# Performance work log

Hardware: AMD Instinct MI355X
Metric: run time of the kernel (lower is better)

## Reference

```python
import jax, jax.numpy as jnp
import numpy as np

SIZE = 896      # GRU hidden size
HALF = SIZE // 2
BINS = 256      # 2**(bits/2), bits=16
B, T = 16, 1000


def _scale(t):
    # [0, BINS-1] ints -> [-1, 1] floats
    return t.astype(jnp.float32) / ((BINS - 1) / 2.0) - 1.0


def setup_inputs() -> dict:
    key = jax.random.key(0)
    ks = jax.random.split(key, 13)
    s = 0.05
    return {
        "conditional": jax.random.normal(ks[0], (B, T, 3, SIZE), jnp.float32),
        "gru_input_bias": jax.random.normal(ks[1], (3 * SIZE,), jnp.float32) * s,
        "W_h": jax.random.normal(ks[2], (3 * SIZE, SIZE), jnp.float32) * s,   # project_hidden
        "b_h": jax.random.normal(ks[3], (3 * SIZE,), jnp.float32) * s,
        "W_ci": jax.random.normal(ks[4], (3 * HALF, 2), jnp.float32) * s,     # project_coarse_input
        "b_ci": jax.random.normal(ks[5], (3 * HALF,), jnp.float32) * s,
        "W_fi": jax.random.normal(ks[6], (3 * HALF, 3), jnp.float32) * s,     # project_fine_input
        "b_fi": jax.random.normal(ks[7], (3 * HALF,), jnp.float32) * s,
        "W_bc": jax.random.normal(ks[8], (BINS, HALF), jnp.float32) * s,      # to_bins_coarse
        "b_bc": jax.random.normal(ks[9], (BINS,), jnp.float32) * s,
        "W_bf": jax.random.normal(ks[10], (BINS, HALF), jnp.float32) * s,     # to_bins_fine
        "b_bf": jax.random.normal(ks[11], (BINS,), jnp.float32) * s,
    }


def reference(conditional, gru_input_bias, W_h, b_h, W_ci, b_ci, W_fi, b_fi,
              W_bc, b_bc, W_bf, b_bf):
    # Fold input-GRU biases into the conditional (as the torch code does in-place)
    cond = conditional + gru_input_bias.reshape(3, SIZE)  # [B,T,3,SIZE]
    # split each gate into coarse/fine halves and regroup as (r,u,e)
    cc = jnp.concatenate([cond[:, :, 0, :HALF], cond[:, :, 1, :HALF], cond[:, :, 2, :HALF]], -1)
    cf = jnp.concatenate([cond[:, :, 0, HALF:], cond[:, :, 1, HALF:], cond[:, :, 2, HALF:]], -1)
    cc = jnp.transpose(cc, (1, 0, 2))  # [T,B,3*HALF]
    cf = jnp.transpose(cf, (1, 0, 2))
    sample_key = jax.random.key(1)

    # initial state: split_signal(0) -> coarse=fine=0 -> scaled to -1
    init = (-jnp.ones((B, 1), jnp.float32), -jnp.ones((B, 1), jnp.float32),
            jnp.zeros((B, HALF), jnp.float32), jnp.zeros((B, HALF), jnp.float32))

    def step(carry, xs):
        cv, fv, ch, fh = carry
        ccond, fcond, t = xs
        k1, k2 = jax.random.split(jax.random.fold_in(sample_key, t))
        hidden = jnp.concatenate([ch, fh], 1)                   # [B,SIZE]
        hp = hidden @ W_h.T + b_h                               # [B,3*SIZE]
        hcr, hfr, hcu, hfu, hce, hfe = jnp.split(hp, 6, axis=1)
        h_cru = jnp.concatenate([hcr, hcu], 1)
        h_fru = jnp.concatenate([hfr, hfu], 1)
        # coarse half-step
        cin = jnp.concatenate([cv, fv], 1)                      # [B,2]
        cp = cin @ W_ci.T + b_ci + ccond                        # [B,3*HALF]
        ru = jax.nn.sigmoid(cp[:, :SIZE] + h_cru)
        r, u = jnp.split(ru, 2, axis=1)
        e = jnp.tanh(r * hce + cp[:, SIZE:])
        ch = u * ch + (1.0 - u) * e
        logits_c = ch @ W_bc.T + b_bc                           # [B,BINS]
        sc = jax.random.categorical(k1, jax.nn.log_softmax(logits_c, axis=1))
        cv = _scale(sc)[:, None]
        # fine half-step
        fin = jnp.concatenate([cin, cv], 1)                     # [B,3]
        fp = fin @ W_fi.T + b_fi + fcond
        ru = jax.nn.sigmoid(fp[:, :SIZE] + h_fru)
        r, u = jnp.split(ru, 2, axis=1)
        e = jnp.tanh(r * hfe + fp[:, SIZE:])
        fh = u * fh + (1.0 - u) * e
        logits_f = fh @ W_bf.T + b_bf
        sf = jax.random.categorical(k2, jax.nn.log_softmax(logits_f, axis=1))
        fv = _scale(sf)[:, None]
        return (cv, fv, ch, fh), (sc, sf)

    (cv, fv, ch, fh), (oc, of) = jax.lax.scan(step, init, (cc, cf, jnp.arange(T)))
    hidden = jnp.concatenate([ch, fh], 1)
    return oc.T, of.T, hidden  # [B,T] int, [B,T] int, [B,SIZE]
```

## Files before the change

kernel.cpp:

```cpp
#include <hip/hip_runtime.h>
#include <stdint.h>

#define BB 16
#define TT 1000
#define SZ 896
#define HF 448
#define NC 112
#define NWG 240
#define LDS_FLOATS 30112
#define LDS_BYTES (LDS_FLOATS * 4)

typedef float f32x4 __attribute__((ext_vector_type(4)));
typedef float f32x2 __attribute__((ext_vector_type(2)));

__device__ float g_hid[2 * BB * SZ];
__device__ float g_hpf4[HF * BB * 4];
__device__ uint32_t g_cdone[NC * 16];
__device__ uint32_t g_fhd[BB * 16];
__device__ uint32_t g_sfd[BB * 16];
__device__ unsigned long long g_afl[BB * 4 * 8];
__device__ unsigned long long g_bfl[BB * 4 * 8];

__device__ __forceinline__ void cload4x4(const float* p, f32x4& a0, f32x4& a1, f32x4& a2, f32x4& a3) {
  asm volatile(
      "global_load_dwordx4 %0, %4, off sc0 sc1\n\t"
      "global_load_dwordx4 %1, %4, off offset:16 sc0 sc1\n\t"
      "global_load_dwordx4 %2, %4, off offset:32 sc0 sc1\n\t"
      "global_load_dwordx4 %3, %4, off offset:48 sc0 sc1\n\t"
      "s_waitcnt vmcnt(0)"
      : "=&v"(a0), "=&v"(a1), "=&v"(a2), "=&v"(a3) : "v"(p) : "memory");
}
__device__ __forceinline__ f32x4 cload1x4(const float* p) {
  f32x4 a;
  asm volatile("global_load_dwordx4 %0, %1, off sc0 sc1\n\ts_waitcnt vmcnt(0)"
               : "=&v"(a) : "v"(p) : "memory");
  return a;
}
__device__ __forceinline__ void cstore1d(float* p, float v) {
  asm volatile("global_store_dword %0, %1, off sc0 sc1\n\ts_waitcnt vmcnt(0)"
               :: "v"(p), "v"(v) : "memory");
}
__device__ __forceinline__ void cstore4d(float* p, f32x4 v) {
  asm volatile("global_store_dwordx4 %0, %1, off sc0 sc1\n\ts_waitcnt vmcnt(0)"
               :: "v"(p), "v"(v) : "memory");
}
__device__ __forceinline__ void cstore1u_nw(uint32_t* p, uint32_t v) {
  asm volatile("global_store_dword %0, %1, off sc0 sc1" :: "v"(p), "v"(v) : "memory");
}
__device__ __forceinline__ void cstore2u_nw(unsigned long long* p, f32x2 v) {
  asm volatile("global_store_dwordx2 %0, %1, off sc0 sc1" :: "v"(p), "v"(v) : "memory");
}

__device__ __forceinline__ void waitFlag(uint32_t* f, uint32_t target) {
  while (__hip_atomic_load(f, __ATOMIC_RELAXED, __HIP_MEMORY_SCOPE_AGENT) < target)
    __builtin_amdgcn_s_sleep(1);
}
__device__ __forceinline__ void waitFlagA(uint32_t* f, uint32_t target) {
  while (__hip_atomic_load(f, __ATOMIC_RELAXED, __HIP_MEMORY_SCOPE_AGENT) < target)
    __builtin_amdgcn_s_sleep(2);
}
__device__ __forceinline__ unsigned long long waitFlag64(unsigned long long* f, uint32_t tag) {
  unsigned long long u;
  while ((uint32_t)((u = __hip_atomic_load(f, __ATOMIC_RELAXED, __HIP_MEMORY_SCOPE_AGENT)) >> 48) < tag)
    __builtin_amdgcn_s_sleep(1);
  return u;
}
__device__ __forceinline__ uint32_t waitFlagHi8(uint32_t* f, uint32_t tag) {
  uint32_t v;
  while (((v = __hip_atomic_load(f, __ATOMIC_RELAXED, __HIP_MEMORY_SCOPE_AGENT)) >> 8) < tag)
    __builtin_amdgcn_s_sleep(1);
  return v;
}

__device__ __forceinline__ uint32_t rotl32(uint32_t v, int d) {
  return (v << d) | (v >> (32 - d));
}

__device__ __forceinline__ uint2 tf2(uint32_t k0, uint32_t k1, uint32_t x0, uint32_t x1) {
  const uint32_t k2 = k0 ^ k1 ^ 0x1BD11BDAu;
  x0 += k0; x1 += k1;
  x0 += x1; x1 = rotl32(x1,13); x1 ^= x0;
  x0 += x1; x1 = rotl32(x1,15); x1 ^= x0;
  x0 += x1; x1 = rotl32(x1,26); x1 ^= x0;
  x0 += x1; x1 = rotl32(x1, 6); x1 ^= x0;
  x0 += k1; x1 += k2 + 1u;
  x0 += x1; x1 = rotl32(x1,17); x1 ^= x0;
  x0 += x1; x1 = rotl32(x1,29); x1 ^= x0;
  x0 += x1; x1 = rotl32(x1,16); x1 ^= x0;
  x0 += x1; x1 = rotl32(x1,24); x1 ^= x0;
  x0 += k2; x1 += k0 + 2u;
  x0 += x1; x1 = rotl32(x1,13); x1 ^= x0;
  x0 += x1; x1 = rotl32(x1,15); x1 ^= x0;
  x0 += x1; x1 = rotl32(x1,26); x1 ^= x0;
  x0 += x1; x1 = rotl32(x1, 6); x1 ^= x0;
  x0 += k0; x1 += k1 + 3u;
  x0 += x1; x1 = rotl32(x1,17); x1 ^= x0;
  x0 += x1; x1 = rotl32(x1,29); x1 ^= x0;
  x0 += x1; x1 = rotl32(x1,16); x1 ^= x0;
  x0 += x1; x1 = rotl32(x1,24); x1 ^= x0;
  x0 += k1; x1 += k2 + 4u;
  x0 += x1; x1 = rotl32(x1,13); x1 ^= x0;
  x0 += x1; x1 = rotl32(x1,15); x1 ^= x0;
  x0 += x1; x1 = rotl32(x1,26); x1 ^= x0;
  x0 += x1; x1 = rotl32(x1, 6); x1 ^= x0;
  x0 += k2; x1 += k0 + 5u;
  return make_uint2(x0, x1);
}

__device__ __forceinline__ float gumbel_bits(uint32_t bits) {
  const float tiny = 1.17549435e-38f;
  float f = __uint_as_float((bits >> 9) | 0x3f800000u) - 1.0f;
  float u = fmaxf(tiny, f + tiny);
  return -logf(-logf(u));
}

__device__ __forceinline__ void logits64(const float* __restrict__ wlds,
                                         const float* __restrict__ vec,
                                         float* __restrict__ plds, int tid) {
  const int w = tid >> 6, lane = tid & 63;
  float a = 0.f;
  const float* wp = wlds + (56 * w) * 65 + lane;
  const float* cp = vec + 56 * w;
#pragma unroll 8
  for (int ii = 0; ii < 56; ++ii)
    a = fmaf(cp[ii], wp[ii * 65], a);
  plds[(w << 6) | lane] = a;
}

__global__ __launch_bounds__(256, 1) void wavernn_init() {
  const int idx = blockIdx.x * 256 + threadIdx.x;
  g_hid[idx] = 0.f;
  if (idx < NC * 16) g_cdone[idx] = 0u;
  if (idx < BB * 16) { g_fhd[idx] = 0u; g_sfd[idx] = 0u; }
  if (idx < BB * 4 * 8) { g_afl[idx] = 0ull; g_bfl[idx] = 0ull; }
}

__global__ __launch_bounds__(512, 1) void wavernn_main(
    const float* __restrict__ cond, const float* __restrict__ gib,
    const float* __restrict__ W_h,  const float* __restrict__ b_h,
    const float* __restrict__ W_ci, const float* __restrict__ b_ci,
    const float* __restrict__ W_fi, const float* __restrict__ b_fi,
    const float* __restrict__ W_bc, const float* __restrict__ b_bc,
    const float* __restrict__ W_bf, const float* __restrict__ b_bf,
    float* __restrict__ out) {
  extern __shared__ float smem[];
  const int wg = blockIdx.x, tid = threadIdx.x;

  if (wg < NC) {
    float* hlds = smem;
    int* smcv = (int*)(smem + 14400);
    int* smfv = (int*)(smem + 14416);
    const int wave = tid >> 6, lane = tid & 63;
    const int l32 = lane >> 1, b2 = lane & 1;
    const int tp = wave >> 2;
    const int chan = (wg << 2) | (wave & 3);
    const int rb = tp ? (HF + chan) : chan;
    float4 w[3][7];
    float brow[3];
#pragma unroll
    for (int r = 0; r < 3; ++r) {
      const int row = r * SZ + rb;
      brow[r] = b_h[row];
#pragma unroll
      for (int m = 0; m < 7; ++m)
        w[r][m] = *(const float4*)&W_h[(size_t)row * SZ + 4 * l32 + 128 * m];
    }
    float wci0[3], wci1[3], bcie[3];
    if (tp == 0) {
#pragma unroll
      for (int g = 0; g < 3; ++g) {
        const int rr = g * HF + chan;
        wci0[g] = W_ci[2 * rr]; wci1[g] = W_ci[2 * rr + 1];
        bcie[g] = b_ci[rr] + gib[g * SZ + chan];
      }
    }
    float pc0 = 0.f, pc1 = 0.f, pc2 = 0.f;
    if (tp == 0 && lane < 16) {
      const size_t base = (((size_t)lane * TT) * 3) * SZ + chan;
      pc0 = cond[base]; pc1 = cond[base + SZ]; pc2 = cond[base + 2 * SZ];
    }
    float chreg = 0.f;
    const int r16 = tid & 15, c28 = tid >> 4;

    for (int t = 0; t < TT; ++t) {
      const int p = (t & 1) ^ 1;
      const int q = t & 1;
      if (tid < NC) waitFlagA(&g_cdone[tid * 16], (uint32_t)t);
      __syncthreads();
      if (c28 < 28) {
        const float* src = g_hid + (size_t)p * BB * SZ + r16 * SZ + c28 * 16;
        f32x4 a0, a1, a2, a3;
        cload4x4(src, a0, a1, a2, a3);
        float* dst = hlds + r16 * 900 + c28 * 16;
        *(f32x4*)(dst) = a0; *(f32x4*)(dst + 4) = a1;
        *(f32x4*)(dst + 8) = a2; *(f32x4*)(dst + 12) = a3;
      }
      __syncthreads();
      float acc[3][8];
#pragma unroll
      for (int r = 0; r < 3; ++r)
#pragma unroll
        for (int i = 0; i < 8; ++i) acc[r][i] = 0.f;
#pragma unroll
      for (int i = 0; i < 8; ++i) {
        const int b = b2 + 2 * i;
        const float* hb = hlds + b * 900 + 4 * l32;
        const float4 h0 = *(const float4*)(hb);
        const float4 h1 = *(const float4*)(hb + 128);
        const float4 h2 = *(const float4*)(hb + 256);
#pragma unroll
        for (int r = 0; r < 3; ++r) {
          float s = acc[r][i];
          s = fmaf(w[r][0].x, h0.x, s); s = fmaf(w[r][0].y, h0.y, s);
          s = fmaf(w[r][0].z, h0.z, s); s = fmaf(w[r][0].w, h0.w, s);
          s = fmaf(w[r][1].x, h1.x, s); s = fmaf(w[r][1].y, h1.y, s);
          s = fmaf(w[r][1].z, h1.z, s); s = fmaf(w[r][1].w, h1.w, s);
          s = fmaf(w[r][2].x, h2.x, s); s = fmaf(w[r][2].y, h2.y, s);
          s = fmaf(w[r][2].z, h2.z, s); s = fmaf(w[r][2].w, h2.w, s);
          acc[r][i] = s;
        }
        if (l32 < 16) {
          const float4 h3 = *(const float4*)(hb + 384);
#pragma unroll
          for (int r = 0; r < 3; ++r) {
            float s = acc[r][i];
            s = fmaf(w[r][3].x, h3.x, s); s = fmaf(w[r][3].y, h3.y, s);
            s = fmaf(w[r][3].z, h3.z, s); s = fmaf(w[r][3].w, h3.w, s);
            acc[r][i] = s;
          }
        }
      }
      if (tid < BB) {
        const uint32_t v = waitFlagHi8(&g_fhd[tid * 16], (uint32_t)t);
        smcv[tid] = (int)(v & 255u);
      }
      __syncthreads();
      if (c28 < 28) {
        const float* src = g_hid + (size_t)p * BB * SZ + r16 * SZ + HF + c28 * 16;
        f32x4 a0, a1, a2, a3;
        cload4x4(src, a0, a1, a2, a3);
        float* dst = hlds + r16 * 900 + HF + c28 * 16;
        *(f32x4*)(dst) = a0; *(f32x4*)(dst + 4) = a1;
        *(f32x4*)(dst + 8) = a2; *(f32x4*)(dst + 12) = a3;
      }
      __syncthreads();
#pragma unroll
      for (int i = 0; i < 8; ++i) {
        const int b = b2 + 2 * i;
        const float* hb = hlds + b * 900 + 4 * l32;
        if (l32 >= 16) {
          const float4 h3 = *(const float4*)(hb + 384);
#pragma unroll
          for (int r = 0; r < 3; ++r) {
            float s = acc[r][i];
            s = fmaf(w[r][3].x, h3.x, s); s = fmaf(w[r][3].y, h3.y, s);
            s = fmaf(w[r][3].z, h3.z, s); s = fmaf(w[r][3].w, h3.w, s);
            acc[r][i] = s;
          }
        }
        const float4 h4 = *(const float4*)(hb + 512);
        const float4 h5 = *(const float4*)(hb + 640);
        const float4 h6 = *(const float4*)(hb + 768);
#pragma unroll
        for (int r = 0; r < 3; ++r) {
          float s = acc[r][i];
          s = fmaf(w[r][4].x, h4.x, s); s = fmaf(w[r][4].y, h4.y, s);
          s = fmaf(w[r][4].z, h4.z, s); s = fmaf(w[r][4].w, h4.w, s);
          s = fmaf(w[r][5].x, h5.x, s); s = fmaf(w[r][5].y, h5.y, s);
          s = fmaf(w[r][5].z, h5.z, s); s = fmaf(w[r][5].w, h5.w, s);
          s = fmaf(w[r][6].x, h6.x, s); s = fmaf(w[r][6].y, h6.y, s);
          s = fmaf(w[r][6].z, h6.z, s); s = fmaf(w[r][6].w, h6.w, s);
          acc[r][i] = s;
        }
      }
#pragma unroll
      for (int r = 0; r < 3; ++r)
#pragma unroll
        for (int i = 0; i < 8; ++i) {
          float v = acc[r][i];
          v += __shfl_xor(v, 2);
          v += __shfl_xor(v, 4);
          v += __shfl_xor(v, 8);
          v += __shfl_xor(v, 16);
          v += __shfl_xor(v, 32);
          acc[r][i] = v;
        }
      if (tid < BB) {
        const uint32_t v = waitFlagHi8(&g_sfd[tid * 16], (uint32_t)t);
        smfv[tid] = (int)(v & 255u);
      }
      __syncthreads();
      if (lane < 16) {
        const int bb = lane, i = lane >> 1;
        const float s0 = acc[0][i] + brow[0];
        const float s1 = acc[1][i] + brow[1];
        const float s2 = acc[2][i] + brow[2];
        if (tp == 0) {
          const float cvv = (float)smcv[bb] / 127.5f - 1.0f;
          const float fvv = (float)smfv[bb] / 127.5f - 1.0f;
          const float cp0 = fmaf(cvv, wci0[0], fmaf(fvv, wci1[0], bcie[0])) + pc0;
          const float cp1 = fmaf(cvv, wci0[1], fmaf(fvv, wci1[1], bcie[1])) + pc1;
          const float cp2 = fmaf(cvv, wci0[2], fmaf(fvv, wci1[2], bcie[2])) + pc2;
          const float rg = 1.f / (1.f + expf(-(cp0 + s0)));
          const float ug = 1.f / (1.f + expf(-(cp1 + s1)));
          const float eg = tanhf(fmaf(rg, s2, cp2));
          const float chn = ug * chreg + (1.f - ug) * eg;
          chreg = chn;
          cstore1d(&g_hid[(size_t)q * BB * SZ + bb * SZ + chan], chn);
        } else {
          f32x4 hv; hv.x = s0; hv.y = s1; hv.z = s2; hv.w = 0.f;
          cstore4d(&g_hpf4[((size_t)chan * 16 + bb) * 4], hv);
        }
      }
      __syncthreads();
      if (tid == 0) cstore1u_nw(&g_cdone[wg * 16], (uint32_t)(t + 1));
      if (tp == 0 && lane < 16 && t + 1 < TT) {
        const size_t base = (((size_t)lane * TT + (t + 1)) * 3) * SZ + chan;
        pc0 = cond[base]; pc1 = cond[base + SZ]; pc2 = cond[base + 2 * SZ];
      }
    }
  } else {
    const int swg = wg - NC;
    const int b = swg >> 3;
    const int role = (swg >> 2) & 1;
    const int k = swg & 3;
    float* wlds = smem;
    float* vlds = smem + 29120;
    float* plds = smem + 29568;
    float* aS = smem + 30080;
    int*   aI = (int*)(smem + 30084);
    float* bS = smem + 30088;
    int*   bI = (int*)(smem + 30092);
    {
      const float* Wm = role ? W_bf : W_bc;
      for (int i = tid; i < HF * 64; i += 512) {
        const int bn = i / HF, kk = i - bn * HF;
        wlds[kk * 65 + bn] = Wm[(size_t)(64 * k + bn) * HF + kk];
      }
    }
    const float* bias = role ? b_bf : b_bc;
    float wf0[3], wf1[3], wf2[3], bfe[3];
    float cp0 = 0.f, cp1 = 0.f, cp2 = 0.f;
    if (role == 1 && tid < HF) {
#pragma unroll
      for (int g = 0; g < 3; ++g) {
        const int rr = g * HF + tid;
        wf0[g] = W_fi[3 * rr]; wf1[g] = W_fi[3 * rr + 1]; wf2[g] = W_fi[3 * rr + 2];
        bfe[g] = b_fi[rr] + gib[g * SZ + HF + tid];
      }
      const size_t cbase = (((size_t)b * TT) * 3) * SZ + HF + tid;
      cp0 = cond[cbase]; cp1 = cond[cbase + SZ]; cp2 = cond[cbase + 2 * SZ];
      vlds[tid] = 0.f;
    }
    __syncthreads();
    float cvO = -1.f, fvO = -1.f;

    for (int t = 0; t < TT; ++t) {
      const int q = t & 1;
      const uint2 kf = tf2(0u, 1u, 0u, (uint32_t)t);
      float gub = 0.f;
      if (tid < 64) {
        const uint2 kk = role ? tf2(kf.x, kf.y, 0u, 1u) : tf2(kf.x, kf.y, 0u, 0u);
        const uint2 o = tf2(kk.x, kk.y, 0u, (uint32_t)(b * 256 + 64 * k + tid));
        gub = gumbel_bits(o.x ^ o.y);
      }
      if (role == 0) {
        if (tid < NC) waitFlag(&g_cdone[tid * 16], (uint32_t)(t + 1));
        __syncthreads();
        if (tid < 112) {
          const f32x4 v = cload1x4(g_hid + (size_t)q * BB * SZ + b * SZ + 4 * tid);
          *(f32x4*)&vlds[4 * tid] = v;
        }
        __syncthreads();
        logits64(wlds, vlds, plds, tid);
        __syncthreads();
        if (tid < 64) {
          const float p0 = plds[tid],       p1 = plds[64 + tid];
          const float p2 = plds[128 + tid], p3 = plds[192 + tid];
          const float p4 = plds[256 + tid], p5 = plds[320 + tid];
          const float p6 = plds[384 + tid], p7 = plds[448 + tid];
          const float sum = ((p0 + p1) + (p2 + p3)) + ((p4 + p5) + (p6 + p7));
          float s = (sum + bias[64 * k + tid]) + gub;
          int idx = 64 * k + tid;
#pragma unroll
          for (int m = 1; m < 64; m <<= 1) {
            const float so = __shfl_xor(s, m);
            const int io = __shfl_xor(idx, m);
            if (so > s || (so == s && io < idx)) { s = so; idx = io; }
          }
          if (tid == 0) {
            f32x2 v; v.x = s;
            v.y = __uint_as_float(((uint32_t)(t + 1) << 16) | ((uint32_t)idx << 8));
            cstore2u_nw(&g_afl[(b * 4 + k) * 8], v);
          }
        }
      } else {
        if (tid < NC) waitFlag(&g_cdone[tid * 16], (uint32_t)(t + 1));
        __syncthreads();
        f32x4 hp = {0.f, 0.f, 0.f, 0.f};
        if (tid < HF) hp = cload1x4(g_hpf4 + ((size_t)tid * 16 + b) * 4);
        if (tid >= 448 && tid < 452) {
          const unsigned long long u = waitFlag64(&g_afl[(b * 4 + (tid - 448)) * 8], (uint32_t)(t + 1));
          aS[tid - 448] = __uint_as_float((uint32_t)u);
          aI[tid - 448] = (int)((u >> 40) & 255u);
        }
        __syncthreads();
        float ms = aS[0]; int sc = aI[0];
#pragma unroll
        for (int m = 1; m < 4; ++m) {
          const float so = aS[m]; const int io = aI[m];
          if (so > ms || (so == ms && io < sc)) { ms = so; sc = io; }
        }
        const float cvNew = (float)sc / 127.5f - 1.0f;
        if (tid < HF) {
          const float fp0 = fmaf(cvO, wf0[0], fmaf(fvO, wf1[0], fmaf(cvNew, wf2[0], bfe[0]))) + cp0;
          const float fp1 = fmaf(cvO, wf0[1], fmaf(fvO, wf1[1], fmaf(cvNew, wf2[1], bfe[1]))) + cp1;
          const float fp2 = fmaf(cvO, wf0[2], fmaf(fvO, wf1[2], fmaf(cvNew, wf2[2], bfe[2]))) + cp2;
          const float fhold = vlds[tid];
          const float rg = 1.f / (1.f + expf(-(fp0 + hp.x)));
          const float ug = 1.f / (1.f + expf(-(fp1 + hp.y)));
          const float eg = tanhf(fmaf(rg, hp.z, fp2));
          vlds[tid] = ug * fhold + (1.f - ug) * eg;
        }
        __syncthreads();
        if (k == 0) {
          if (tid < 112)
            cstore4d(&g_hid[(size_t)q * BB * SZ + b * SZ + HF + 4 * tid], *(f32x4*)&vlds[4 * tid]);
          __syncthreads();
          if (tid == 0) cstore1u_nw(&g_fhd[b * 16], ((uint32_t)(t + 1) << 8) | (uint32_t)sc);
        }
        logits64(wlds, vlds, plds, tid);
        __syncthreads();
        if (tid < 64) {
          const float p0 = plds[tid],       p1 = plds[64 + tid];
          const float p2 = plds[128 + tid], p3 = plds[192 + tid];
          const float p4 = plds[256 + tid], p5 = plds[320 + tid];
          const float p6 = plds[384 + tid], p7 = plds[448 + tid];
          const float sum = ((p0 + p1) + (p2 + p3)) + ((p4 + p5) + (p6 + p7));
          float s = (sum + bias[64 * k + tid]) + gub;
          int idx = 64 * k + tid;
#pragma unroll
          for (int m = 1; m < 64; m <<= 1) {
            const float so = __shfl_xor(s, m);
            const int io = __shfl_xor(idx, m);
            if (so > s || (so == s && io < idx)) { s = so; idx = io; }
          }
          if (tid == 0) {
            f32x2 v; v.x = s;
            v.y = __uint_as_float(((uint32_t)(t + 1) << 16) | ((uint32_t)idx << 8));
            cstore2u_nw(&g_bfl[(b * 4 + k) * 8], v);
          }
        }
        if (tid >= 448 && tid < 452) {
          const unsigned long long u = waitFlag64(&g_bfl[(b * 4 + (tid - 448)) * 8], (uint32_t)(t + 1));
          bS[tid - 448] = __uint_as_float((uint32_t)u);
          bI[tid - 448] = (int)((u >> 40) & 255u);
        }
        __syncthreads();
        float msf = bS[0]; int sf = bI[0];
#pragma unroll
        for (int m = 1; m < 4; ++m) {
          const float so = bS[m]; const int io = bI[m];
          if (so > msf || (so == msf && io < sf)) { msf = so; sf = io; }
        }
        if (k == 0 && tid == 0) {
          out[b * TT + t] = (float)sc;
          out[BB * TT + b * TT + t] = (float)sf;
          cstore1u_nw(&g_sfd[b * 16], ((uint32_t)(t + 1) << 8) | (uint32_t)sf);
        }
        cvO = cvNew; fvO = (float)sf / 127.5f - 1.0f;
        if (tid < HF && t + 1 < TT) {
          const size_t cbase = (((size_t)b * TT + (t + 1)) * 3) * SZ + HF + tid;
          cp0 = cond[cbase]; cp1 = cond[cbase + SZ]; cp2 = cond[cbase + 2 * SZ];
        }
      }
    }
    if (k == 0) {
      if (role == 0) {
        if (tid < HF) out[2 * BB * TT + (size_t)b * SZ + tid] = vlds[tid];
      } else {
        if (tid < HF) out[2 * BB * TT + (size_t)b * SZ + HF + tid] = vlds[tid];
      }
    }
  }
}

extern "C" void kernel_launch(void* const* d_in, const int* in_sizes, int n_in,
                              void* d_out, int out_size, void* d_ws, size_t ws_size,
                              hipStream_t stream) {
  (void)in_sizes; (void)n_in; (void)out_size; (void)d_ws; (void)ws_size;
  const float* cond = (const float*)d_in[0];
  const float* gib  = (const float*)d_in[1];
  const float* W_h  = (const float*)d_in[2];
  const float* b_h  = (const float*)d_in[3];
  const float* W_ci = (const float*)d_in[4];
  const float* b_ci = (const float*)d_in[5];
  const float* W_fi = (const float*)d_in[6];
  const float* b_fi = (const float*)d_in[7];
  const float* W_bc = (const float*)d_in[8];
  const float* b_bc = (const float*)d_in[9];
  const float* W_bf = (const float*)d_in[10];
  const float* b_bf = (const float*)d_in[11];
  float* out = (float*)d_out;
  static int attr_done = 0;
  (void)attr_done;
  hipFuncSetAttribute((const void*)wavernn_main,
                      hipFuncAttributeMaxDynamicSharedMemorySize, LDS_BYTES);
  wavernn_init<<<NC, 256, 0, stream>>>();
  wavernn_main<<<NWG, 512, LDS_BYTES, stream>>>(cond, gib, W_h, b_h, W_ci, b_ci,
                                                W_fi, b_fi, W_bc, b_bc, W_bf, b_bf, out);
}
```

Baseline: 12.15 ms.

## Move coarse GRU gate update from matvec workgroups into per-batch coarse-sampling workgroups

The coarse hidden-state gate math moves out of the hidden-projection workgroups and into the per-batch coarse-role workgroups, mirroring the fine path. Projection workgroups now only write pre-activations (g_hpc4/g_hpf4) and signal completion. They no longer wait for the sampled coarse and fine values each step, which removes a dependency from the critical chain. Coarse workgroups now read the previous fine sample from the fine argmax flags and publish the coarse hidden state through a new per-batch ready flag. The cost is more cross-workgroup flag traffic and more coordination inside the sampling workgroups.

```diff
diff --git a/kernel.cpp b/kernel.cpp
--- a/kernel.cpp
+++ b/kernel.cpp
@@ -14,10 +14,11 @@
 typedef float f32x2 __attribute__((ext_vector_type(2)));
 
 __device__ float g_hid[2 * BB * SZ];
-__device__ float g_hpf4[HF * BB * 4];
+__device__ float g_hpc4[BB * HF * 4];
+__device__ float g_hpf4[BB * HF * 4];
 __device__ uint32_t g_cdone[NC * 16];
-__device__ uint32_t g_fhd[BB * 16];
-__device__ uint32_t g_sfd[BB * 16];
+__device__ uint32_t g_chrdy[BB * 16];
+__device__ uint32_t g_fhrdy[BB * 16];
 __device__ unsigned long long g_afl[BB * 4 * 8];
 __device__ unsigned long long g_bfl[BB * 4 * 8];
 
@@ -36,10 +37,6 @@
                : "=&v"(a) : "v"(p) : "memory");
   return a;
 }
-__device__ __forceinline__ void cstore1d(float* p, float v) {
-  asm volatile("global_store_dword %0, %1, off sc0 sc1\n\ts_waitcnt vmcnt(0)"
-               :: "v"(p), "v"(v) : "memory");
-}
 __device__ __forceinline__ void cstore4d(float* p, f32x4 v) {
   asm volatile("global_store_dwordx4 %0, %1, off sc0 sc1\n\ts_waitcnt vmcnt(0)"
                :: "v"(p), "v"(v) : "memory");
@@ -64,12 +61,6 @@
   while ((uint32_t)((u = __hip_atomic_load(f, __ATOMIC_RELAXED, __HIP_MEMORY_SCOPE_AGENT)) >> 48) < tag)
     __builtin_amdgcn_s_sleep(1);
   return u;
-}
-__device__ __forceinline__ uint32_t waitFlagHi8(uint32_t* f, uint32_t tag) {
-  uint32_t v;
-  while (((v = __hip_atomic_load(f, __ATOMIC_RELAXED, __HIP_MEMORY_SCOPE_AGENT)) >> 8) < tag)
-    __builtin_amdgcn_s_sleep(1);
-  return v;
 }
 
 __device__ __forceinline__ uint32_t rotl32(uint32_t v, int d) {
@@ -131,7 +122,7 @@
   const int idx = blockIdx.x * 256 + threadIdx.x;
   g_hid[idx] = 0.f;
   if (idx < NC * 16) g_cdone[idx] = 0u;
-  if (idx < BB * 16) { g_fhd[idx] = 0u; g_sfd[idx] = 0u; }
+  if (idx < BB * 16) { g_chrdy[idx] = 0u; g_fhrdy[idx] = 0u; }
   if (idx < BB * 4 * 8) { g_afl[idx] = 0ull; g_bfl[idx] = 0ull; }
 }
 
@@ -148,8 +139,6 @@
 
   if (wg < NC) {
     float* hlds = smem;
-    int* smcv = (int*)(smem + 14400);
-    int* smfv = (int*)(smem + 14416);
     const int wave = tid >> 6, lane = tid & 63;
     const int l32 = lane >> 1, b2 = lane & 1;
     const int tp = wave >> 2;
@@ -165,27 +154,11 @@
       for (int m = 0; m < 7; ++m)
         w[r][m] = *(const float4*)&W_h[(size_t)row * SZ + 4 * l32 + 128 * m];
     }
-    float wci0[3], wci1[3], bcie[3];
-    if (tp == 0) {
-#pragma unroll
-      for (int g = 0; g < 3; ++g) {
-        const int rr = g * HF + chan;
-        wci0[g] = W_ci[2 * rr]; wci1[g] = W_ci[2 * rr + 1];
-        bcie[g] = b_ci[rr] + gib[g * SZ + chan];
-      }
-    }
-    float pc0 = 0.f, pc1 = 0.f, pc2 = 0.f;
-    if (tp == 0 && lane < 16) {
-      const size_t base = (((size_t)lane * TT) * 3) * SZ + chan;
-      pc0 = cond[base]; pc1 = cond[base + SZ]; pc2 = cond[base + 2 * SZ];
-    }
-    float chreg = 0.f;
     const int r16 = tid & 15, c28 = tid >> 4;
 
     for (int t = 0; t < TT; ++t) {
       const int p = (t & 1) ^ 1;
-      const int q = t & 1;
-      if (tid < NC) waitFlagA(&g_cdone[tid * 16], (uint32_t)t);
+      if (tid < BB) waitFlagA(&g_chrdy[tid * 16], (uint32_t)t);
       __syncthreads();
       if (c28 < 28) {
         const float* src = g_hid + (size_t)p * BB * SZ + r16 * SZ + c28 * 16;
@@ -230,10 +203,7 @@
           }
         }
       }
-      if (tid < BB) {
-        const uint32_t v = waitFlagHi8(&g_fhd[tid * 16], (uint32_t)t);
-        smcv[tid] = (int)(v & 255u);
-      }
+      if (tid < BB) waitFlag(&g_fhrdy[tid * 16], (uint32_t)t);
       __syncthreads();
       if (c28 < 28) {
         const float* src = g_hid + (size_t)p * BB * SZ + r16 * SZ + HF + c28 * 16;
@@ -285,39 +255,18 @@
           v += __shfl_xor(v, 32);
           acc[r][i] = v;
         }
-      if (tid < BB) {
-        const uint32_t v = waitFlagHi8(&g_sfd[tid * 16], (uint32_t)t);
-        smfv[tid] = (int)(v & 255u);
-      }
-      __syncthreads();
       if (lane < 16) {
         const int bb = lane, i = lane >> 1;
-        const float s0 = acc[0][i] + brow[0];
-        const float s1 = acc[1][i] + brow[1];
-        const float s2 = acc[2][i] + brow[2];
-        if (tp == 0) {
-          const float cvv = (float)smcv[bb] / 127.5f - 1.0f;
-          const float fvv = (float)smfv[bb] / 127.5f - 1.0f;
-          const float cp0 = fmaf(cvv, wci0[0], fmaf(fvv, wci1[0], bcie[0])) + pc0;
-          const float cp1 = fmaf(cvv, wci0[1], fmaf(fvv, wci1[1], bcie[1])) + pc1;
-          const float cp2 = fmaf(cvv, wci0[2], fmaf(fvv, wci1[2], bcie[2])) + pc2;
-          const float rg = 1.f / (1.f + expf(-(cp0 + s0)));
-          const float ug = 1.f / (1.f + expf(-(cp1 + s1)));
-          const float eg = tanhf(fmaf(rg, s2, cp2));
-          const float chn = ug * chreg + (1.f - ug) * eg;
-          chreg = chn;
-          cstore1d(&g_hid[(size_t)q * BB * SZ + bb * SZ + chan], chn);
-        } else {
-          f32x4 hv; hv.x = s0; hv.y = s1; hv.z = s2; hv.w = 0.f;
-          cstore4d(&g_hpf4[((size_t)chan * 16 + bb) * 4], hv);
-        }
+        f32x4 hv;
+        hv.x = acc[0][i] + brow[0];
+        hv.y = acc[1][i] + brow[1];
+        hv.z = acc[2][i] + brow[2];
+        hv.w = 0.f;
+        float* dst = (tp ? g_hpf4 : g_hpc4) + ((size_t)bb * HF + chan) * 4;
+        cstore4d(dst, hv);
       }
       __syncthreads();
       if (tid == 0) cstore1u_nw(&g_cdone[wg * 16], (uint32_t)(t + 1));
-      if (tp == 0 && lane < 16 && t + 1 < TT) {
-        const size_t base = (((size_t)lane * TT + (t + 1)) * 3) * SZ + chan;
-        pc0 = cond[base]; pc1 = cond[base + SZ]; pc2 = cond[base + 2 * SZ];
-      }
     }
   } else {
     const int swg = wg - NC;
@@ -339,21 +288,30 @@
       }
     }
     const float* bias = role ? b_bf : b_bc;
-    float wf0[3], wf1[3], wf2[3], bfe[3];
-    float cp0 = 0.f, cp1 = 0.f, cp2 = 0.f;
-    if (role == 1 && tid < HF) {
-#pragma unroll
-      for (int g = 0; g < 3; ++g) {
-        const int rr = g * HF + tid;
-        wf0[g] = W_fi[3 * rr]; wf1[g] = W_fi[3 * rr + 1]; wf2[g] = W_fi[3 * rr + 2];
-        bfe[g] = b_fi[rr] + gib[g * SZ + HF + tid];
-      }
-      const size_t cbase = (((size_t)b * TT) * 3) * SZ + HF + tid;
-      cp0 = cond[cbase]; cp1 = cond[cbase + SZ]; cp2 = cond[cbase + 2 * SZ];
+    float gw0[3], gw1[3], gw2[3], gbe[3], pc[3];
+    if (tid < HF) {
+      if (role == 0) {
+#pragma unroll
+        for (int g = 0; g < 3; ++g) {
+          const int rr = g * HF + tid;
+          gw0[g] = W_ci[2 * rr]; gw1[g] = W_ci[2 * rr + 1]; gw2[g] = 0.f;
+          gbe[g] = b_ci[rr] + gib[g * SZ + tid];
+          pc[g] = cond[(((size_t)b * TT) * 3 + g) * SZ + tid];
+        }
+      } else {
+#pragma unroll
+        for (int g = 0; g < 3; ++g) {
+          const int rr = g * HF + tid;
+          gw0[g] = W_fi[3 * rr]; gw1[g] = W_fi[3 * rr + 1]; gw2[g] = W_fi[3 * rr + 2];
+          gbe[g] = b_fi[rr] + gib[g * SZ + HF + tid];
+          pc[g] = cond[(((size_t)b * TT) * 3 + g) * SZ + HF + tid];
+        }
+      }
       vlds[tid] = 0.f;
     }
     __syncthreads();
-    float cvO = -1.f, fvO = -1.f;
+    float cvO = -1.f;
+    float fvO = -1.f;
 
     for (int t = 0; t < TT; ++t) {
       const int q = t & 1;
@@ -365,13 +323,40 @@
         gub = gumbel_bits(o.x ^ o.y);
       }
       if (role == 0) {
+        if (t > 0 && tid >= 452 && tid < 456) {
+          const unsigned long long u = waitFlag64(&g_bfl[(b * 4 + (tid - 452)) * 8], (uint32_t)t);
+          bS[tid - 452] = __uint_as_float((uint32_t)u);
+          bI[tid - 452] = (int)((u >> 40) & 255u);
+        }
         if (tid < NC) waitFlag(&g_cdone[tid * 16], (uint32_t)(t + 1));
         __syncthreads();
-        if (tid < 112) {
-          const f32x4 v = cload1x4(g_hid + (size_t)q * BB * SZ + b * SZ + 4 * tid);
-          *(f32x4*)&vlds[4 * tid] = v;
-        }
-        __syncthreads();
+        float fvv = -1.f;
+        if (t > 0) {
+          float ms = bS[0]; int sf = bI[0];
+#pragma unroll
+          for (int m = 1; m < 4; ++m) {
+            const float so = bS[m]; const int io = bI[m];
+            if (so > ms || (so == ms && io < sf)) { ms = so; sf = io; }
+          }
+          fvv = (float)sf / 127.5f - 1.0f;
+        }
+        if (tid < HF) {
+          const f32x4 hp = cload1x4(&g_hpc4[((size_t)b * HF + tid) * 4]);
+          const float cp0 = fmaf(cvO, gw0[0], fmaf(fvv, gw1[0], gbe[0])) + pc[0];
+          const float cp1 = fmaf(cvO, gw0[1], fmaf(fvv, gw1[1], gbe[1])) + pc[1];
+          const float cp2 = fmaf(cvO, gw0[2], fmaf(fvv, gw1[2], gbe[2])) + pc[2];
+          const float rg = 1.f / (1.f + expf(-(cp0 + hp.x)));
+          const float ug = 1.f / (1.f + expf(-(cp1 + hp.y)));
+          const float eg = tanhf(fmaf(rg, hp.z, cp2));
+          vlds[tid] = ug * vlds[tid] + (1.f - ug) * eg;
+        }
+        __syncthreads();
+        if (k == 0) {
+          if (tid < 112)
+            cstore4d(&g_hid[(size_t)q * BB * SZ + b * SZ + 4 * tid], *(f32x4*)&vlds[4 * tid]);
+          __syncthreads();
+          if (tid == 0) cstore1u_nw(&g_chrdy[b * 16], (uint32_t)(t + 1));
+        }
         logits64(wlds, vlds, plds, tid);
         __syncthreads();
         if (tid < 64) {
@@ -394,17 +379,38 @@
             cstore2u_nw(&g_afl[(b * 4 + k) * 8], v);
           }
         }
-      } else {
-        if (tid < NC) waitFlag(&g_cdone[tid * 16], (uint32_t)(t + 1));
-        __syncthreads();
-        f32x4 hp = {0.f, 0.f, 0.f, 0.f};
-        if (tid < HF) hp = cload1x4(g_hpf4 + ((size_t)tid * 16 + b) * 4);
         if (tid >= 448 && tid < 452) {
           const unsigned long long u = waitFlag64(&g_afl[(b * 4 + (tid - 448)) * 8], (uint32_t)(t + 1));
           aS[tid - 448] = __uint_as_float((uint32_t)u);
           aI[tid - 448] = (int)((u >> 40) & 255u);
         }
         __syncthreads();
+        {
+          float ms = aS[0]; int sc = aI[0];
+#pragma unroll
+          for (int m = 1; m < 4; ++m) {
+            const float so = aS[m]; const int io = aI[m];
+            if (so > ms || (so == ms && io < sc)) { ms = so; sc = io; }
+          }
+          cvO = (float)sc / 127.5f - 1.0f;
+          if (k == 0 && tid == 0) out[b * TT + t] = (float)sc;
+        }
+        if (tid < HF && t + 1 < TT) {
+#pragma unroll
+          for (int g = 0; g < 3; ++g)
+            pc[g] = cond[(((size_t)b * TT + (t + 1)) * 3 + g) * SZ + tid];
+        }
+      } else {
+        if (tid < NC) waitFlag(&g_cdone[tid * 16], (uint32_t)(t + 1));
+        __syncthreads();
+        f32x4 hp = {0.f, 0.f, 0.f, 0.f};
+        if (tid < HF) hp = cload1x4(&g_hpf4[((size_t)b * HF + tid) * 4]);
+        if (tid >= 448 && tid < 452) {
+          const unsigned long long u = waitFlag64(&g_afl[(b * 4 + (tid - 448)) * 8], (uint32_t)(t + 1));
+          aS[tid - 448] = __uint_as_float((uint32_t)u);
+          aI[tid - 448] = (int)((u >> 40) & 255u);
+        }
+        __syncthreads();
         float ms = aS[0]; int sc = aI[0];
 #pragma unroll
         for (int m = 1; m < 4; ++m) {
@@ -413,21 +419,20 @@
         }
         const float cvNew = (float)sc / 127.5f - 1.0f;
         if (tid < HF) {
-          const float fp0 = fmaf(cvO, wf0[0], fmaf(fvO, wf1[0], fmaf(cvNew, wf2[0], bfe[0]))) + cp0;
-          const float fp1 = fmaf(cvO, wf0[1], fmaf(fvO, wf1[1], fmaf(cvNew, wf2[1], bfe[1]))) + cp1;
-          const float fp2 = fmaf(cvO, wf0[2], fmaf(fvO, wf1[2], fmaf(cvNew, wf2[2], bfe[2]))) + cp2;
-          const float fhold = vlds[tid];
+          const float fp0 = fmaf(cvO, gw0[0], fmaf(fvO, gw1[0], fmaf(cvNew, gw2[0], gbe[0]))) + pc[0];
+          const float fp1 = fmaf(cvO, gw0[1], fmaf(fvO, gw1[1], fmaf(cvNew, gw2[1], gbe[1]))) + pc[1];
+          const float fp2 = fmaf(cvO, gw0[2], fmaf(fvO, gw1[2], fmaf(cvNew, gw2[2], gbe[2]))) + pc[2];
           const float rg = 1.f / (1.f + expf(-(fp0 + hp.x)));
           const float ug = 1.f / (1.f + expf(-(fp1 + hp.y)));
           const float eg = tanhf(fmaf(rg, hp.z, fp2));
-          vlds[tid] = ug * fhold + (1.f - ug) * eg;
+          vlds[tid] = ug * vlds[tid] + (1.f - ug) * eg;
         }
         __syncthreads();
         if (k == 0) {
           if (tid < 112)
             cstore4d(&g_hid[(size_t)q * BB * SZ + b * SZ + HF + 4 * tid], *(f32x4*)&vlds[4 * tid]);
           __syncthreads();
-          if (tid == 0) cstore1u_nw(&g_fhd[b * 16], ((uint32_t)(t + 1) << 8) | (uint32_t)sc);
+          if (tid == 0) cstore1u_nw(&g_fhrdy[b * 16], (uint32_t)(t + 1));
         }
         logits64(wlds, vlds, plds, tid);
         __syncthreads();
@@ -457,30 +462,27 @@
           bI[tid - 448] = (int)((u >> 40) & 255u);
         }
         __syncthreads();
-        float msf = bS[0]; int sf = bI[0];
-#pragma unroll
-        for (int m = 1; m < 4; ++m) {
-          const float so = bS[m]; const int io = bI[m];
-          if (so > msf || (so == msf && io < sf)) { msf = so; sf = io; }
-        }
-        if (k == 0 && tid == 0) {
-          out[b * TT + t] = (float)sc;
-          out[BB * TT + b * TT + t] = (float)sf;
-          cstore1u_nw(&g_sfd[b * 16], ((uint32_t)(t + 1) << 8) | (uint32_t)sf);
-        }
-        cvO = cvNew; fvO = (float)sf / 127.5f - 1.0f;
+        {
+          float msf = bS[0]; int sf = bI[0];
+#pragma unroll
+          for (int m = 1; m < 4; ++m) {
+            const float so = bS[m]; const int io = bI[m];
+            if (so > msf || (so == msf && io < sf)) { msf = so; sf = io; }
+          }
+          fvO = (float)sf / 127.5f - 1.0f;
+          if (k == 0 && tid == 0) out[BB * TT + b * TT + t] = (float)sf;
+        }
+        cvO = cvNew;
         if (tid < HF && t + 1 < TT) {
-          const size_t cbase = (((size_t)b * TT + (t + 1)) * 3) * SZ + HF + tid;
-          cp0 = cond[cbase]; cp1 = cond[cbase + SZ]; cp2 = cond[cbase + 2 * SZ];
+#pragma unroll
+          for (int g = 0; g < 3; ++g)
+            pc[g] = cond[(((size_t)b * TT + (t + 1)) * 3 + g) * SZ + HF + tid];
         }
       }
     }
-    if (k == 0) {
-      if (role == 0) {
-        if (tid < HF) out[2 * BB * TT + (size_t)b * SZ + tid] = vlds[tid];
-      } else {
-        if (tid < HF) out[2 * BB * TT + (size_t)b * SZ + HF + tid] = vlds[tid];
-      }
+    if (k == 0 && tid < HF) {
+      if (role == 0) out[2 * BB * TT + (size_t)b * SZ + tid] = vlds[tid];
+      else           out[2 * BB * TT + (size_t)b * SZ + HF + tid] = vlds[tid];
     }
   }
 }
@@ -502,8 +504,6 @@
   const float* W_bf = (const float*)d_in[10];
   const float* b_bf = (const float*)d_in[11];
   float* out = (float*)d_out;
-  static int attr_done = 0;
-  (void)attr_done;
   hipFuncSetAttribute((const void*)wavernn_main,
                       hipFuncAttributeMaxDynamicSharedMemorySize, LDS_BYTES);
   wavernn_init<<<NC, 256, 0, stream>>>();
```

After: 13.01 ms. +7.1%, slower.
